# Optimization experiments

Hardware: AMD Instinct MI355X
Metric: run time of the kernel (lower is better)

## Reference

```python
import jax, jax.numpy as jnp
import numpy as np

B, T, D = 16, 4096, 512
N_SLOTS = 64


def setup_inputs() -> dict:
    key = jax.random.key(0)
    ks = jax.random.split(key, 7)
    s = 1.0 / np.sqrt(D)  # keep tanh out of deep saturation, like orthogonal*0.9 init
    return {
        "x_seq": jax.random.normal(ks[0], (B, T, D), jnp.float32),
        "h_tape": jax.random.normal(ks[1], (B, N_SLOTS, D), jnp.float32) * 0.1,
        "h_work": jax.random.normal(ks[2], (B, D), jnp.float32) * 0.1,
        "W_h": jax.random.normal(ks[3], (D, D), jnp.float32) * s,
        "W_x": jax.random.normal(ks[4], (D, D), jnp.float32) * s,
        "b_h": jnp.zeros((D,), jnp.float32),
        "W_write": jax.random.normal(ks[5], (D, D), jnp.float32) * s,
    }


def reference(x_seq, h_tape, h_work, W_h, W_x, b_h, W_write):
    """Dual-memory Elman recurrence.

    Per step t:
      read_t  = softmax(h_tape @ h_work / sqrt(D)) @ h_tape   (content-based tape read)
      h_work  = tanh(W_h h_work + W_x x_t + read_t + b_h)
      tape write: slot (t mod n_slots) <- W_write h_work      (FIFO tape write)
    Returns (h_work_out [B,T,D], h_tape_final [B,S,D], last h_work [B,D]).
    """
    scale = jnp.asarray(1.0 / np.sqrt(D), x_seq.dtype)

    def step(carry, inp):
        tape, h = carry
        x_t, t = inp
        scores = jnp.einsum("bsd,bd->bs", tape, h) * scale        # [B,S]
        attn = jax.nn.softmax(scores, axis=-1)
        read = jnp.einsum("bs,bsd->bd", attn, tape)               # [B,D]
        h_new = jnp.tanh(h @ W_h.T + x_t @ W_x.T + read + b_h)    # [B,D]
        w_vec = h_new @ W_write.T                                 # [B,D]
        slot = t % N_SLOTS
        tape = jax.lax.dynamic_update_slice(tape, w_vec[:, None, :], (0, slot, 0))
        return (tape, h_new), h_new

    xs = (jnp.swapaxes(x_seq, 0, 1), jnp.arange(x_seq.shape[1]))
    (tape_f, _), h_seq = jax.lax.scan(step, (h_tape, h_work), xs)
    h_work_out = jnp.swapaxes(h_seq, 0, 1)  # [B,T,D]
    return h_work_out, tape_f, h_work_out[:, -1]
```

## Files before the change

kernel.cpp:

```cpp
#include <hip/hip_runtime.h>
#include <cstddef>

#define B_SZ   16
#define T_SZ   4096
#define D_SZ   512
#define NSLOT  64
#define NW     16
#define RPW    32
#define TP     36
#define SCALE  0.044194173824159216f

__device__ __align__(8) unsigned long long g_pb[B_SZ * NW * NSLOT];
__device__ __align__(8) unsigned long long g_hb[B_SZ * D_SZ];
__device__ __align__(8) unsigned long long g_q [B_SZ * NW];

#define AL(p)    __hip_atomic_load((p),  __ATOMIC_RELAXED, __HIP_MEMORY_SCOPE_AGENT)
#define AS(p,v)  __hip_atomic_store((p), (v), __ATOMIC_RELAXED, __HIP_MEMORY_SCOPE_AGENT)

__device__ __forceinline__ unsigned long long pk(float v, unsigned tag) {
    return ((unsigned long long)tag << 32) | (unsigned long long)__float_as_uint(v);
}
__device__ __forceinline__ float lo(unsigned long long v) {
    return __uint_as_float((unsigned)v);
}

__global__ __launch_bounds__(256)
void xw_gemm_kernel(const float* __restrict__ X, const float* __restrict__ Wx,
                    const float* __restrict__ bh, float* __restrict__ out)
{
    __shared__ float As[16][68];
    __shared__ float Bs[16][68];
    const int m0 = blockIdx.x * 64;
    const int n0 = blockIdx.y * 64;
    const int tid = threadIdx.x;
    const int tr = tid >> 4, tc = tid & 15;
    const int lrow = tid >> 2;
    const int lkk  = (tid & 3) * 4;

    float acc[4][4] = {};

    for (int k0 = 0; k0 < D_SZ; k0 += 16) {
        float4 av = *(const float4*)(X  + (size_t)(m0 + lrow) * D_SZ + k0 + lkk);
        float4 bv = *(const float4*)(Wx + (size_t)(n0 + lrow) * D_SZ + k0 + lkk);
        As[lkk+0][lrow] = av.x; As[lkk+1][lrow] = av.y;
        As[lkk+2][lrow] = av.z; As[lkk+3][lrow] = av.w;
        Bs[lkk+0][lrow] = bv.x; Bs[lkk+1][lrow] = bv.y;
        Bs[lkk+2][lrow] = bv.z; Bs[lkk+3][lrow] = bv.w;
        __syncthreads();
        #pragma unroll
        for (int kk = 0; kk < 16; ++kk) {
            float a[4], b[4];
            #pragma unroll
            for (int i = 0; i < 4; ++i) a[i] = As[kk][tr*4+i];
            #pragma unroll
            for (int j = 0; j < 4; ++j) b[j] = Bs[kk][tc*4+j];
            #pragma unroll
            for (int i = 0; i < 4; ++i)
                #pragma unroll
                for (int j = 0; j < 4; ++j)
                    acc[i][j] = fmaf(a[i], b[j], acc[i][j]);
        }
        __syncthreads();
    }
    #pragma unroll
    for (int i = 0; i < 4; ++i) {
        const int m = m0 + tr*4 + i;
        const int n = n0 + tc*4;
        float4 o;
        o.x = acc[i][0] + bh[n+0];
        o.y = acc[i][1] + bh[n+1];
        o.z = acc[i][2] + bh[n+2];
        o.w = acc[i][3] + bh[n+3];
        *(float4*)(out + (size_t)m * D_SZ + n) = o;
    }
}

__global__ __launch_bounds__(256, 1)
void recurrence_mw(const float* __restrict__ tape0, const float* __restrict__ h0,
                   const float* __restrict__ W_h, const float* __restrict__ W_w,
                   float* __restrict__ out)
{
    __shared__ __align__(16) float tp[NSLOT][TP];
    __shared__ __align__(16) float hh[D_SZ];
    __shared__ __align__(16) float hno[RPW];
    __shared__ float scr[NSLOT];
    __shared__ float es[NSLOT];
    __shared__ float zmv[RPW];
    __shared__ float rp8[8][RPW];
    __shared__ float sml[2];

    const int blk = blockIdx.x;
    const int xcd = blk & 7;
    const int jj0 = blk >> 3;
    const int b   = xcd * 2 + (jj0 & 1);
    const int w   = jj0 >> 1;
    const int R0  = w * RPW;
    const int tid = threadIdx.x;
    const int fb  = b * NW;
    const int g16 = tid >> 4, sj = tid & 15;
    const int sA  = tid >> 2, qA = tid & 3;
    const int sg  = tid >> 5, jB = tid & 31;

    if (tid < NSLOT) AS(&g_pb[((size_t)fb + w) * NSLOT + tid], 0ULL);
    if (tid < RPW)   AS(&g_hb[(size_t)b * D_SZ + R0 + tid], 0ULL);
    if (tid == 0)    AS(&g_q[fb + w], 0ULL);

    float4 wh0[8], wh1[8], ww0[8], ww1[8];
    {
        const float* a0 = W_h + (size_t)(R0 + g16)      * D_SZ + 4 * sj;
        const float* a1 = W_h + (size_t)(R0 + g16 + 16) * D_SZ + 4 * sj;
        const float* b0 = W_w + (size_t)(R0 + g16)      * D_SZ + 4 * sj;
        const float* b1 = W_w + (size_t)(R0 + g16 + 16) * D_SZ + 4 * sj;
        #pragma unroll
        for (int i = 0; i < 8; ++i) {
            wh0[i] = *(const float4*)(a0 + 64 * i);
            wh1[i] = *(const float4*)(a1 + 64 * i);
            ww0[i] = *(const float4*)(b0 + 64 * i);
            ww1[i] = *(const float4*)(b1 + 64 * i);
        }
    }

    for (int i = tid; i < NSLOT * RPW; i += 256) {
        const int s = i >> 5, j = i & 31;
        tp[s][j] = tape0[((size_t)b * NSLOT + s) * D_SZ + R0 + j];
    }
    for (int i = tid; i < D_SZ; i += 256) hh[i] = h0[(size_t)b * D_SZ + i];
    __syncthreads();

    float* outb = out + (size_t)b * T_SZ * D_SZ;

    if (tid < RPW) {
        hno[tid] = hh[R0 + tid];
        AS(&g_hb[(size_t)b * D_SZ + R0 + tid], pk(hh[R0 + tid], 1u));
    }
    __syncthreads();
    {
        const float* trow = &tp[sA][8 * qA];
        float4 t0 = *(const float4*)trow;
        float4 t1 = *(const float4*)(trow + 4);
        float4 h0v = *(const float4*)&hno[8 * qA];
        float4 h1v = *(const float4*)&hno[8 * qA + 4];
        float pp = t0.x*h0v.x + t0.y*h0v.y + t0.z*h0v.z + t0.w*h0v.w
                 + t1.x*h1v.x + t1.y*h1v.y + t1.z*h1v.z + t1.w*h1v.w;
        pp += __shfl_xor(pp, 1);
        pp += __shfl_xor(pp, 2);
        if (qA == 0) AS(&g_pb[((size_t)fb + w) * NSLOT + sA], pk(pp, 1u));
    }

    for (int t = 0; t < T_SZ; ++t) {
        const unsigned tgB = (unsigned)(t + 1);
        const int sp = (t - 1) & 63;

        float xwv = 0.f;
        if (tid < RPW) xwv = outb[(size_t)t * D_SZ + R0 + tid];
        {
            const unsigned long long* pb = &g_pb[((size_t)fb + qA * 4) * NSLOT + sA];
            const unsigned long long* hb = &g_hb[(size_t)b * D_SZ + 2 * tid];
            unsigned long long p0, p1, p2, p3, v0, v1;
            for (;;) {
                p0 = AL(pb);              p1 = AL(pb + NSLOT);
                p2 = AL(pb + 2 * NSLOT);  p3 = AL(pb + 3 * NSLOT);
                v0 = AL(hb);              v1 = AL(hb + 1);
                if ((unsigned)(p0 >> 32) == tgB && (unsigned)(p1 >> 32) == tgB &&
                    (unsigned)(p2 >> 32) == tgB && (unsigned)(p3 >> 32) == tgB &&
                    (unsigned)(v0 >> 32) == tgB && (unsigned)(v1 >> 32) == tgB) break;
                __builtin_amdgcn_s_sleep(1);
            }
            float s4 = lo(p0) + lo(p1) + lo(p2) + lo(p3);
            s4 += __shfl_xor(s4, 1);
            s4 += __shfl_xor(s4, 2);
            if (qA == 0) scr[sA] = s4 * SCALE;
            hh[2 * tid]     = lo(v0);
            hh[2 * tid + 1] = lo(v1);
        }
        __syncthreads();

        {
            float z0 = 0.f, z1 = 0.f, v0 = 0.f, v1 = 0.f;
            #pragma unroll
            for (int i = 0; i < 8; ++i) {
                float4 hr = *(const float4*)&hh[4 * sj + 64 * i];
                z0 = fmaf(wh0[i].x, hr.x, z0); z0 = fmaf(wh0[i].y, hr.y, z0);
                z0 = fmaf(wh0[i].z, hr.z, z0); z0 = fmaf(wh0[i].w, hr.w, z0);
                z1 = fmaf(wh1[i].x, hr.x, z1); z1 = fmaf(wh1[i].y, hr.y, z1);
                z1 = fmaf(wh1[i].z, hr.z, z1); z1 = fmaf(wh1[i].w, hr.w, z1);
                v0 = fmaf(ww0[i].x, hr.x, v0); v0 = fmaf(ww0[i].y, hr.y, v0);
                v0 = fmaf(ww0[i].z, hr.z, v0); v0 = fmaf(ww0[i].w, hr.w, v0);
                v1 = fmaf(ww1[i].x, hr.x, v1); v1 = fmaf(ww1[i].y, hr.y, v1);
                v1 = fmaf(ww1[i].z, hr.z, v1); v1 = fmaf(ww1[i].w, hr.w, v1);
            }
            #pragma unroll
            for (int o = 1; o <= 8; o <<= 1) {
                z0 += __shfl_xor(z0, o); z1 += __shfl_xor(z1, o);
                v0 += __shfl_xor(v0, o); v1 += __shfl_xor(v1, o);
            }
            if (sj == 0) {
                zmv[g16] = z0; zmv[g16 + 16] = z1;
                if (t > 0) { tp[sp][g16] = v0; tp[sp][g16 + 16] = v1; }
            }
        }
        __syncthreads();

        if (tid < 64) {
            const float v = (t > 0 && tid == sp) ? -3.0e38f : scr[tid];
            float m = v;
            #pragma unroll
            for (int o = 32; o; o >>= 1) m = fmaxf(m, __shfl_xor(m, o));
            const float e = __expf(v - m);
            float s = e;
            #pragma unroll
            for (int o = 32; o; o >>= 1) s += __shfl_xor(s, o);
            es[tid] = e;
            if (tid == 0) { sml[0] = m; sml[1] = s; }
        } else if (tid < 96 && t > 0) {
            const int ld = tid - 64;
            float qp = tp[sp][ld] * hh[R0 + ld];
            #pragma unroll
            for (int o = 1; o <= 16; o <<= 1) qp += __shfl_xor(qp, o);
            if (ld == 0) AS(&g_q[fb + w], pk(qp, tgB));
        }
        __syncthreads();

        {
            float acc = 0.f;
            #pragma unroll
            for (int s8 = 0; s8 < 8; ++s8)
                acc = fmaf(es[sg * 8 + s8], tp[sg * 8 + s8][jB], acc);
            rp8[sg][jB] = acc;
        }
        __syncthreads();

        if (tid < RPW) {
            const float rr = rp8[0][tid] + rp8[1][tid] + rp8[2][tid] + rp8[3][tid]
                           + rp8[4][tid] + rp8[5][tid] + rp8[6][tid] + rp8[7][tid];
            float rd;
            if (t > 0) {
                const unsigned long long* qp_ = &g_q[fb + (tid & 15)];
                unsigned long long qv;
                for (;;) {
                    qv = AL(qp_);
                    if ((unsigned)(qv >> 32) == tgB) break;
                    __builtin_amdgcn_s_sleep(1);
                }
                float qs = lo(qv);
                qs += __shfl_xor(qs, 1); qs += __shfl_xor(qs, 2);
                qs += __shfl_xor(qs, 4); qs += __shfl_xor(qs, 8);
                const float esig = __expf(qs * SCALE - sml[0]);
                rd = (rr + esig * tp[sp][tid]) / (sml[1] + esig);
            } else {
                rd = rr / sml[1];
            }
            const float hn = tanhf(zmv[tid] + rd + xwv);
            outb[(size_t)t * D_SZ + R0 + tid] = hn;
            AS(&g_hb[(size_t)b * D_SZ + R0 + tid], pk(hn, (unsigned)(t + 2)));
            hno[tid] = hn;
        }
        __syncthreads();

        {
            const float* trow = &tp[sA][8 * qA];
            float4 t0 = *(const float4*)trow;
            float4 t1 = *(const float4*)(trow + 4);
            float4 h0v = *(const float4*)&hno[8 * qA];
            float4 h1v = *(const float4*)&hno[8 * qA + 4];
            float pp = t0.x*h0v.x + t0.y*h0v.y + t0.z*h0v.z + t0.w*h0v.w
                     + t1.x*h1v.x + t1.y*h1v.y + t1.z*h1v.z + t1.w*h1v.w;
            pp += __shfl_xor(pp, 1);
            pp += __shfl_xor(pp, 2);
            if (qA == 0) AS(&g_pb[((size_t)fb + w) * NSLOT + sA], pk(pp, (unsigned)(t + 2)));
        }
    }

    {
        const unsigned long long* hb = &g_hb[(size_t)b * D_SZ + 2 * tid];
        unsigned long long v0, v1;
        const unsigned tgF = (unsigned)(T_SZ + 1);
        for (;;) {
            v0 = AL(hb); v1 = AL(hb + 1);
            if ((unsigned)(v0 >> 32) == tgF && (unsigned)(v1 >> 32) == tgF) break;
            __builtin_amdgcn_s_sleep(1);
        }
        hh[2 * tid]     = lo(v0);
        hh[2 * tid + 1] = lo(v1);
    }
    __syncthreads();
    {
        float v0 = 0.f, v1 = 0.f;
        #pragma unroll
        for (int i = 0; i < 8; ++i) {
            float4 hr = *(const float4*)&hh[4 * sj + 64 * i];
            v0 = fmaf(ww0[i].x, hr.x, v0); v0 = fmaf(ww0[i].y, hr.y, v0);
            v0 = fmaf(ww0[i].z, hr.z, v0); v0 = fmaf(ww0[i].w, hr.w, v0);
            v1 = fmaf(ww1[i].x, hr.x, v1); v1 = fmaf(ww1[i].y, hr.y, v1);
            v1 = fmaf(ww1[i].z, hr.z, v1); v1 = fmaf(ww1[i].w, hr.w, v1);
        }
        #pragma unroll
        for (int o = 1; o <= 8; o <<= 1) { v0 += __shfl_xor(v0, o); v1 += __shfl_xor(v1, o); }
        if (sj == 0) { tp[63][g16] = v0; tp[63][g16 + 16] = v1; }
    }
    __syncthreads();
    float* tout = out + (size_t)B_SZ * T_SZ * D_SZ + (size_t)b * NSLOT * D_SZ;
    for (int i = tid; i < NSLOT * RPW; i += 256) {
        const int s = i >> 5, j = i & 31;
        tout[(size_t)s * D_SZ + R0 + j] = tp[s][j];
    }
    if (w == 0) {
        float* lout = out + (size_t)B_SZ * T_SZ * D_SZ
                          + (size_t)B_SZ * NSLOT * D_SZ + (size_t)b * D_SZ;
        for (int i = tid; i < D_SZ; i += 256) lout[i] = hh[i];
    }
}

extern "C" void kernel_launch(void* const* d_in, const int* in_sizes, int n_in,
                              void* d_out, int out_size, void* d_ws, size_t ws_size,
                              hipStream_t stream)
{
    const float* x_seq   = (const float*)d_in[0];
    const float* h_tape  = (const float*)d_in[1];
    const float* h_work  = (const float*)d_in[2];
    const float* W_h     = (const float*)d_in[3];
    const float* W_x     = (const float*)d_in[4];
    const float* b_h     = (const float*)d_in[5];
    const float* W_write = (const float*)d_in[6];
    float* out = (float*)d_out;

    dim3 g1(T_SZ * B_SZ / 64, D_SZ / 64);
    xw_gemm_kernel<<<g1, 256, 0, stream>>>(x_seq, W_x, b_h, out);

    recurrence_mw<<<B_SZ * NW, 256, 0, stream>>>(h_tape, h_work, W_h, W_write, out);
}
```

Baseline: 18.40 ms.

## Add fast-path mirrored flag buffers with raw-asm polling and fallback

Duplicates every inter-block handoff buffer into mirror arrays that are written with plain global stores and polled with sc0 loads plus explicit waitcnt, with no sleep between polls. Each poll has an iteration budget, and on timeout it falls back permanently to the original relaxed atomic path. It also stops keeping the W_h and W_write slices in registers and reloads them from global memory every step, which frees registers but adds per-step memory traffic. The goal is to cut cross-block synchronisation latency, at the cost of doubled flag stores and possible memory-ordering and visibility hazards.

Result: slower. 21.81 ms (+18.6%).

```diff
diff --git a/kernel.cpp b/kernel.cpp
--- a/kernel.cpp
+++ b/kernel.cpp
@@ -13,6 +13,9 @@
 __device__ __align__(8) unsigned long long g_pb[B_SZ * NW * NSLOT];
 __device__ __align__(8) unsigned long long g_hb[B_SZ * D_SZ];
 __device__ __align__(8) unsigned long long g_q [B_SZ * NW];
+__device__ __align__(8) unsigned long long g_pbF[B_SZ * NW * NSLOT];
+__device__ __align__(8) unsigned long long g_hbF[B_SZ * D_SZ];
+__device__ __align__(8) unsigned long long g_qF [B_SZ * NW];
 
 #define AL(p)    __hip_atomic_load((p),  __ATOMIC_RELAXED, __HIP_MEMORY_SCOPE_AGENT)
 #define AS(p,v)  __hip_atomic_store((p), (v), __ATOMIC_RELAXED, __HIP_MEMORY_SCOPE_AGENT)
@@ -23,6 +26,16 @@
 __device__ __forceinline__ float lo(unsigned long long v) {
     return __uint_as_float((unsigned)v);
 }
+__device__ __forceinline__ void FS(unsigned long long* p, unsigned long long v) {
+    asm volatile("global_store_dwordx2 %0, %1, off" :: "v"(p), "v"(v) : "memory");
+}
+__device__ __forceinline__ unsigned long long FL(const unsigned long long* p) {
+    unsigned long long v;
+    asm volatile("global_load_dwordx2 %0, %1, off sc0" : "=v"(v) : "v"(p) : "memory");
+    return v;
+}
+#define VM0_SB() do { asm volatile("s_waitcnt vmcnt(0)" ::: "memory"); \
+                      __builtin_amdgcn_sched_barrier(0); } while (0)
 
 __global__ __launch_bounds__(256)
 void xw_gemm_kernel(const float* __restrict__ X, const float* __restrict__ Wx,
@@ -49,16 +62,16 @@
         __syncthreads();
         #pragma unroll
         for (int kk = 0; kk < 16; ++kk) {
-            float a[4], b[4];
+            float a[4], bq[4];
             #pragma unroll
             for (int i = 0; i < 4; ++i) a[i] = As[kk][tr*4+i];
             #pragma unroll
-            for (int j = 0; j < 4; ++j) b[j] = Bs[kk][tc*4+j];
+            for (int j = 0; j < 4; ++j) bq[j] = Bs[kk][tc*4+j];
             #pragma unroll
             for (int i = 0; i < 4; ++i)
                 #pragma unroll
                 for (int j = 0; j < 4; ++j)
-                    acc[i][j] = fmaf(a[i], b[j], acc[i][j]);
+                    acc[i][j] = fmaf(a[i], bq[j], acc[i][j]);
         }
         __syncthreads();
     }
@@ -101,24 +114,15 @@
     const int sA  = tid >> 2, qA = tid & 3;
     const int sg  = tid >> 5, jB = tid & 31;
 
-    if (tid < NSLOT) AS(&g_pb[((size_t)fb + w) * NSLOT + tid], 0ULL);
-    if (tid < RPW)   AS(&g_hb[(size_t)b * D_SZ + R0 + tid], 0ULL);
-    if (tid == 0)    AS(&g_q[fb + w], 0ULL);
-
-    float4 wh0[8], wh1[8], ww0[8], ww1[8];
-    {
-        const float* a0 = W_h + (size_t)(R0 + g16)      * D_SZ + 4 * sj;
-        const float* a1 = W_h + (size_t)(R0 + g16 + 16) * D_SZ + 4 * sj;
-        const float* b0 = W_w + (size_t)(R0 + g16)      * D_SZ + 4 * sj;
-        const float* b1 = W_w + (size_t)(R0 + g16 + 16) * D_SZ + 4 * sj;
-        #pragma unroll
-        for (int i = 0; i < 8; ++i) {
-            wh0[i] = *(const float4*)(a0 + 64 * i);
-            wh1[i] = *(const float4*)(a1 + 64 * i);
-            ww0[i] = *(const float4*)(b0 + 64 * i);
-            ww1[i] = *(const float4*)(b1 + 64 * i);
-        }
-    }
+    if (tid < NSLOT) {
+        AS(&g_pb [((size_t)fb + w) * NSLOT + tid], 0ULL);
+        FS(&g_pbF[((size_t)fb + w) * NSLOT + tid], 0ULL);
+    }
+    if (tid < RPW) {
+        AS(&g_hb [(size_t)b * D_SZ + R0 + tid], 0ULL);
+        FS(&g_hbF[(size_t)b * D_SZ + R0 + tid], 0ULL);
+    }
+    if (tid == 0) { AS(&g_q[fb + w], 0ULL); FS(&g_qF[fb + w], 0ULL); }
 
     for (int i = tid; i < NSLOT * RPW; i += 256) {
         const int s = i >> 5, j = i & 31;
@@ -131,7 +135,9 @@
 
     if (tid < RPW) {
         hno[tid] = hh[R0 + tid];
-        AS(&g_hb[(size_t)b * D_SZ + R0 + tid], pk(hh[R0 + tid], 1u));
+        const unsigned long long v = pk(hh[R0 + tid], 1u);
+        FS(&g_hbF[(size_t)b * D_SZ + R0 + tid], v);
+        AS(&g_hb [(size_t)b * D_SZ + R0 + tid], v);
     }
     __syncthreads();
     {
@@ -144,8 +150,14 @@
                  + t1.x*h1v.x + t1.y*h1v.y + t1.z*h1v.z + t1.w*h1v.w;
         pp += __shfl_xor(pp, 1);
         pp += __shfl_xor(pp, 2);
-        if (qA == 0) AS(&g_pb[((size_t)fb + w) * NSLOT + sA], pk(pp, 1u));
-    }
+        if (qA == 0) {
+            const unsigned long long v = pk(pp, 1u);
+            FS(&g_pbF[((size_t)fb + w) * NSLOT + sA], v);
+            AS(&g_pb [((size_t)fb + w) * NSLOT + sA], v);
+        }
+    }
+
+    bool fast0 = true, fastq = true;
 
     for (int t = 0; t < T_SZ; ++t) {
         const unsigned tgB = (unsigned)(t + 1);
@@ -154,17 +166,38 @@
         float xwv = 0.f;
         if (tid < RPW) xwv = outb[(size_t)t * D_SZ + R0 + tid];
         {
-            const unsigned long long* pb = &g_pb[((size_t)fb + qA * 4) * NSLOT + sA];
-            const unsigned long long* hb = &g_hb[(size_t)b * D_SZ + 2 * tid];
+            const unsigned long long* pbS = &g_pb [((size_t)fb + qA * 4) * NSLOT + sA];
+            const unsigned long long* hbS = &g_hb [(size_t)b * D_SZ + 2 * tid];
+            const unsigned long long* pbF = &g_pbF[((size_t)fb + qA * 4) * NSLOT + sA];
+            const unsigned long long* hbF = &g_hbF[(size_t)b * D_SZ + 2 * tid];
             unsigned long long p0, p1, p2, p3, v0, v1;
-            for (;;) {
-                p0 = AL(pb);              p1 = AL(pb + NSLOT);
-                p2 = AL(pb + 2 * NSLOT);  p3 = AL(pb + 3 * NSLOT);
-                v0 = AL(hb);              v1 = AL(hb + 1);
-                if ((unsigned)(p0 >> 32) == tgB && (unsigned)(p1 >> 32) == tgB &&
-                    (unsigned)(p2 >> 32) == tgB && (unsigned)(p3 >> 32) == tgB &&
-                    (unsigned)(v0 >> 32) == tgB && (unsigned)(v1 >> 32) == tgB) break;
-                __builtin_amdgcn_s_sleep(1);
+            bool got = false;
+            if (fast0) {
+                int budget = (t == 0) ? 1200 : 200;
+                for (;;) {
+                    p0 = FL(pbF);             p1 = FL(pbF + NSLOT);
+                    p2 = FL(pbF + 2 * NSLOT); p3 = FL(pbF + 3 * NSLOT);
+                    v0 = FL(hbF);             v1 = FL(hbF + 1);
+                    VM0_SB();
+                    if ((unsigned)(p0 >> 32) == tgB && (unsigned)(p1 >> 32) == tgB &&
+                        (unsigned)(p2 >> 32) == tgB && (unsigned)(p3 >> 32) == tgB &&
+                        (unsigned)(v0 >> 32) == tgB && (unsigned)(v1 >> 32) == tgB) {
+                        got = true; break;
+                    }
+                    if (--budget <= 0) break;
+                }
+                if (!got) fast0 = false;
+            }
+            if (!got) {
+                for (;;) {
+                    p0 = AL(pbS);              p1 = AL(pbS + NSLOT);
+                    p2 = AL(pbS + 2 * NSLOT);  p3 = AL(pbS + 3 * NSLOT);
+                    v0 = AL(hbS);              v1 = AL(hbS + 1);
+                    if ((unsigned)(p0 >> 32) == tgB && (unsigned)(p1 >> 32) == tgB &&
+                        (unsigned)(p2 >> 32) == tgB && (unsigned)(p3 >> 32) == tgB &&
+                        (unsigned)(v0 >> 32) == tgB && (unsigned)(v1 >> 32) == tgB) break;
+                    __builtin_amdgcn_s_sleep(1);
+                }
             }
             float s4 = lo(p0) + lo(p1) + lo(p2) + lo(p3);
             s4 += __shfl_xor(s4, 1);
@@ -177,17 +210,25 @@
 
         {
             float z0 = 0.f, z1 = 0.f, v0 = 0.f, v1 = 0.f;
+            const float* whA = W_h + (size_t)(R0 + g16)      * D_SZ + 4 * sj;
+            const float* whB = W_h + (size_t)(R0 + g16 + 16) * D_SZ + 4 * sj;
+            const float* wwA = W_w + (size_t)(R0 + g16)      * D_SZ + 4 * sj;
+            const float* wwB = W_w + (size_t)(R0 + g16 + 16) * D_SZ + 4 * sj;
             #pragma unroll
             for (int i = 0; i < 8; ++i) {
                 float4 hr = *(const float4*)&hh[4 * sj + 64 * i];
-                z0 = fmaf(wh0[i].x, hr.x, z0); z0 = fmaf(wh0[i].y, hr.y, z0);
-                z0 = fmaf(wh0[i].z, hr.z, z0); z0 = fmaf(wh0[i].w, hr.w, z0);
-                z1 = fmaf(wh1[i].x, hr.x, z1); z1 = fmaf(wh1[i].y, hr.y, z1);
-                z1 = fmaf(wh1[i].z, hr.z, z1); z1 = fmaf(wh1[i].w, hr.w, z1);
-                v0 = fmaf(ww0[i].x, hr.x, v0); v0 = fmaf(ww0[i].y, hr.y, v0);
-                v0 = fmaf(ww0[i].z, hr.z, v0); v0 = fmaf(ww0[i].w, hr.w, v0);
-                v1 = fmaf(ww1[i].x, hr.x, v1); v1 = fmaf(ww1[i].y, hr.y, v1);
-                v1 = fmaf(ww1[i].z, hr.z, v1); v1 = fmaf(ww1[i].w, hr.w, v1);
+                float4 a0 = *(const float4*)(whA + 64 * i);
+                float4 a1 = *(const float4*)(whB + 64 * i);
+                float4 b0 = *(const float4*)(wwA + 64 * i);
+                float4 b1 = *(const float4*)(wwB + 64 * i);
+                z0 = fmaf(a0.x, hr.x, z0); z0 = fmaf(a0.y, hr.y, z0);
+                z0 = fmaf(a0.z, hr.z, z0); z0 = fmaf(a0.w, hr.w, z0);
+                z1 = fmaf(a1.x, hr.x, z1); z1 = fmaf(a1.y, hr.y, z1);
+                z1 = fmaf(a1.z, hr.z, z1); z1 = fmaf(a1.w, hr.w, z1);
+                v0 = fmaf(b0.x, hr.x, v0); v0 = fmaf(b0.y, hr.y, v0);
+                v0 = fmaf(b0.z, hr.z, v0); v0 = fmaf(b0.w, hr.w, v0);
+                v1 = fmaf(b1.x, hr.x, v1); v1 = fmaf(b1.y, hr.y, v1);
+                v1 = fmaf(b1.z, hr.z, v1); v1 = fmaf(b1.w, hr.w, v1);
             }
             #pragma unroll
             for (int o = 1; o <= 8; o <<= 1) {
@@ -217,7 +258,11 @@
             float qp = tp[sp][ld] * hh[R0 + ld];
             #pragma unroll
             for (int o = 1; o <= 16; o <<= 1) qp += __shfl_xor(qp, o);
-            if (ld == 0) AS(&g_q[fb + w], pk(qp, tgB));
+            if (ld == 0) {
+                const unsigned long long v = pk(qp, tgB);
+                FS(&g_qF[fb + w], v);
+                AS(&g_q [fb + w], v);
+            }
         }
         __syncthreads();
 
@@ -235,12 +280,26 @@
                            + rp8[4][tid] + rp8[5][tid] + rp8[6][tid] + rp8[7][tid];
             float rd;
             if (t > 0) {
-                const unsigned long long* qp_ = &g_q[fb + (tid & 15)];
+                const unsigned long long* qS = &g_q [fb + (tid & 15)];
+                const unsigned long long* qF = &g_qF[fb + (tid & 15)];
                 unsigned long long qv;
-                for (;;) {
-                    qv = AL(qp_);
-                    if ((unsigned)(qv >> 32) == tgB) break;
-                    __builtin_amdgcn_s_sleep(1);
+                bool got = false;
+                if (fastq) {
+                    int budget = (t == 1) ? 1200 : 200;
+                    for (;;) {
+                        qv = FL(qF);
+                        VM0_SB();
+                        if ((unsigned)(qv >> 32) == tgB) { got = true; break; }
+                        if (--budget <= 0) break;
+                    }
+                    if (!got) fastq = false;
+                }
+                if (!got) {
+                    for (;;) {
+                        qv = AL(qS);
+                        if ((unsigned)(qv >> 32) == tgB) break;
+                        __builtin_amdgcn_s_sleep(1);
+                    }
                 }
                 float qs = lo(qv);
                 qs += __shfl_xor(qs, 1); qs += __shfl_xor(qs, 2);
@@ -252,7 +311,9 @@
             }
             const float hn = tanhf(zmv[tid] + rd + xwv);
             outb[(size_t)t * D_SZ + R0 + tid] = hn;
-            AS(&g_hb[(size_t)b * D_SZ + R0 + tid], pk(hn, (unsigned)(t + 2)));
+            const unsigned long long v = pk(hn, (unsigned)(t + 2));
+            FS(&g_hbF[(size_t)b * D_SZ + R0 + tid], v);
+            AS(&g_hb [(size_t)b * D_SZ + R0 + tid], v);
             hno[tid] = hn;
         }
         __syncthreads();
@@ -267,7 +328,11 @@
                      + t1.x*h1v.x + t1.y*h1v.y + t1.z*h1v.z + t1.w*h1v.w;
             pp += __shfl_xor(pp, 1);
             pp += __shfl_xor(pp, 2);
-            if (qA == 0) AS(&g_pb[((size_t)fb + w) * NSLOT + sA], pk(pp, (unsigned)(t + 2)));
+            if (qA == 0) {
+                const unsigned long long v = pk(pp, (unsigned)(t + 2));
+                FS(&g_pbF[((size_t)fb + w) * NSLOT + sA], v);
+                AS(&g_pb [((size_t)fb + w) * NSLOT + sA], v);
+            }
         }
     }
 
@@ -286,13 +351,17 @@
     __syncthreads();
     {
         float v0 = 0.f, v1 = 0.f;
+        const float* wwA = W_w + (size_t)(R0 + g16)      * D_SZ + 4 * sj;
+        const float* wwB = W_w + (size_t)(R0 + g16 + 16) * D_SZ + 4 * sj;
         #pragma unroll
         for (int i = 0; i < 8; ++i) {
             float4 hr = *(const float4*)&hh[4 * sj + 64 * i];
-            v0 = fmaf(ww0[i].x, hr.x, v0); v0 = fmaf(ww0[i].y, hr.y, v0);
-            v0 = fmaf(ww0[i].z, hr.z, v0); v0 = fmaf(ww0[i].w, hr.w, v0);
-            v1 = fmaf(ww1[i].x, hr.x, v1); v1 = fmaf(ww1[i].y, hr.y, v1);
-            v1 = fmaf(ww1[i].z, hr.z, v1); v1 = fmaf(ww1[i].w, hr.w, v1);
+            float4 b0 = *(const float4*)(wwA + 64 * i);
+            float4 b1 = *(const float4*)(wwB + 64 * i);
+            v0 = fmaf(b0.x, hr.x, v0); v0 = fmaf(b0.y, hr.y, v0);
+            v0 = fmaf(b0.z, hr.z, v0); v0 = fmaf(b0.w, hr.w, v0);
+            v1 = fmaf(b1.x, hr.x, v1); v1 = fmaf(b1.y, hr.y, v1);
+            v1 = fmaf(b1.z, hr.z, v1); v1 = fmaf(b1.w, hr.w, v1);
         }
         #pragma unroll
         for (int o = 1; o <= 8; o <<= 1) { v0 += __shfl_xor(v0, o); v1 += __shfl_xor(v1, o); }
```
